# Performance work log

Measured on AMD Instinct MI355X. Metric: run time of the kernel, lower is better.

Reference implementation:

```python
import jax
import jax.numpy as jnp
from jax import lax
import numpy as np

E = 4          # num_experts
CIN = 128
COUT = 128
K = 3
STAT = 6
HID = 16       # router hidden width
STRIDE = 1
PAD = 1


def setup_inputs() -> dict:
    key = jax.random.key(0)
    ks = jax.random.split(key, 8)
    B, H, W = 32, 64, 64
    x = jax.random.normal(ks[0], (B, CIN, H, W), dtype=jnp.float32)
    scene_stats = jax.random.normal(ks[1], (B, STAT), dtype=jnp.float32)
    # router: Linear(stat_dim,16) -> ReLU -> Linear(16,E) -> Softmax
    W1 = jax.random.normal(ks[2], (HID, STAT), dtype=jnp.float32) * (1.0 / np.sqrt(STAT))
    b1 = jnp.zeros((HID,), dtype=jnp.float32)
    W2 = jax.random.normal(ks[3], (E, HID), dtype=jnp.float32) * (1.0 / np.sqrt(HID))
    b2 = jnp.zeros((E,), dtype=jnp.float32)
    weight_experts = jax.random.normal(ks[4], (E, COUT, CIN, K, K), dtype=jnp.float32) * 0.02
    bias_experts = jnp.zeros((E, COUT), dtype=jnp.float32)
    return {"x": x, "scene_stats": scene_stats, "W1": W1, "b1": b1,
            "W2": W2, "b2": b2, "weight_experts": weight_experts,
            "bias_experts": bias_experts}


def reference(x, scene_stats, W1, b1, W2, b2, weight_experts, bias_experts):
    B, Cin, H, W = x.shape
    Cout = weight_experts.shape[1]
    # router
    h = jax.nn.relu(scene_stats @ W1.T + b1)                 # [B, HID]
    routing = jax.nn.softmax(h @ W2.T + b2, axis=1)          # [B, E]
    # per-sample dynamic weights / bias
    dyn_w = jnp.einsum('bk,koihw->boihw', routing, weight_experts)  # [B,Cout,Cin,K,K]
    dyn_b = jnp.einsum('bk,ko->bo', routing, bias_experts)          # [B,Cout]
    # grouped conv with groups = B (each sample uses its own filter bank)
    x_r = x.reshape(1, B * Cin, H, W)
    w_r = dyn_w.reshape(B * Cout, Cin, K, K)
    out = lax.conv_general_dilated(
        x_r, w_r,
        window_strides=(STRIDE, STRIDE),
        padding=((PAD, PAD), (PAD, PAD)),
        feature_group_count=B,
        dimension_numbers=('NCHW', 'OIHW', 'NCHW'))
    out = out.reshape(B, Cout, out.shape[2], out.shape[3])
    return out + dyn_b[:, :, None, None]
```

## Files before the change

kernel.cpp:

```cpp
#include <hip/hip_runtime.h>
#include <hip/hip_bf16.h>


typedef short bf16x8 __attribute__((ext_vector_type(8)));
typedef float f32x4  __attribute__((ext_vector_type(4)));
typedef unsigned u32x4 __attribute__((ext_vector_type(4)));

#define VMWAIT(n) asm volatile("s_waitcnt vmcnt(" #n ")" ::: "memory")
#define LGKM0()   asm volatile("s_waitcnt lgkmcnt(0)" ::: "memory")

static __device__ __forceinline__ unsigned short f2bf(float f) {
    unsigned u = __float_as_uint(f);
    u = u + 0x7FFFu + ((u >> 16) & 1u);
    return (unsigned short)(u >> 16);
}

static __device__ __forceinline__ void gl2lds16(const unsigned short* g, unsigned short* l) {
    __builtin_amdgcn_global_load_lds(
        (const __attribute__((address_space(1))) unsigned int*)g,
        (__attribute__((address_space(3))) unsigned int*)l,
        16, 0, 0);
}

__global__ void prep_kernel(const float* __restrict__ stats, const float* __restrict__ W1,
                            const float* __restrict__ b1, const float* __restrict__ W2,
                            const float* __restrict__ b2, const float* __restrict__ wexp,
                            const float* __restrict__ bexp, unsigned short* __restrict__ dynw,
                            float* __restrict__ dynb)
{
    __shared__ float ls[4*1152];
    __shared__ float lr[32*4];
    const int tid = threadIdx.x;
    const int co  = blockIdx.x & 127;
    const int bg  = blockIdx.x >> 7;

    if (tid < 32) {
        float s[6];
#pragma unroll
        for (int i = 0; i < 6; ++i) s[i] = stats[tid*6 + i];
        float h[16];
#pragma unroll
        for (int j = 0; j < 16; ++j) {
            float a = b1[j];
#pragma unroll
            for (int i = 0; i < 6; ++i) a += W1[j*6+i]*s[i];
            h[j] = a > 0.f ? a : 0.f;
        }
        float lg[4];
#pragma unroll
        for (int e = 0; e < 4; ++e) {
            float a = b2[e];
#pragma unroll
            for (int j = 0; j < 16; ++j) a += W2[e*16+j]*h[j];
            lg[e] = a;
        }
        float m = fmaxf(fmaxf(lg[0],lg[1]), fmaxf(lg[2],lg[3]));
        float ex[4], sum = 0.f;
#pragma unroll
        for (int e = 0; e < 4; ++e) { ex[e] = expf(lg[e]-m); sum += ex[e]; }
        float inv = 1.f / sum;
#pragma unroll
        for (int e = 0; e < 4; ++e) lr[tid*4+e] = ex[e]*inv;
    }
    for (int i = tid; i < 4*1152; i += 256) {
        int e = i / 1152, j = i - e*1152;
        ls[i] = wexp[((unsigned long long)(e*128 + co))*1152 + j];
    }
    __syncthreads();

    if (bg == 0 && tid < 32) {
        float sb = 0.f;
#pragma unroll
        for (int e = 0; e < 4; ++e) sb += lr[tid*4+e] * bexp[e*128 + co];
        dynb[tid*128 + co] = sb;
    }

    const int ci  = tid & 127;
    const int tp0 = tid >> 7;
    const int cic = ci >> 5;
    const int g   = (ci >> 3) & 3;
    const int jj  = ci & 7;
    const int mi  = co >> 4;
    const int l15 = co & 15;
    for (int bb = bg*8; bb < bg*8 + 8; ++bb) {
        float r0 = lr[bb*4+0], r1 = lr[bb*4+1], r2 = lr[bb*4+2], r3 = lr[bb*4+3];
#pragma unroll
        for (int pp = 0; pp < 5; ++pp) {
            int tap = 2*pp + tp0;
            if (tap < 9) {
                int j = ci*9 + tap;
                float v = r0*ls[j] + r1*ls[1152+j] + r2*ls[2*1152+j] + r3*ls[3*1152+j];
                dynw[((((unsigned long long)(bb*4 + cic)*9 + tap)*8 + mi)*64 + g*16 + l15)*8 + jj] = f2bf(v);
            }
        }
    }
}

__global__ __launch_bounds__(256, 2) void conv_kernel(
    const float* __restrict__ x,
    const unsigned short* __restrict__ dynw,
    const float* __restrict__ dynb,
    float* __restrict__ out)
{
    __shared__ __align__(16) unsigned short xs[6*16*136];
    __shared__ __align__(16) unsigned short wsm[6][4096];

    const int tid  = threadIdx.x;
    const int wave = tid >> 6;
    const int lane = tid & 63;
    const int l15  = lane & 15;
    const int g    = lane >> 4;
    const int pr   = tid >> 4;
    const int c4   = tid & 15;

    int bidx = ((blockIdx.x & 7) << 6) | (blockIdx.x >> 3);
    const int b  = bidx >> 4;
    const int r0 = (bidx & 15) << 2;

    f32x4 acc[8][4];
#pragma unroll
    for (int mi = 0; mi < 8; ++mi)
#pragma unroll
        for (int ni = 0; ni < 4; ++ni) acc[mi][ni] = (f32x4){0.f,0.f,0.f,0.f};

    const float* xsrcb = x + (unsigned long long)b*(128ull*64*64);
    const unsigned short* wsrcb = dynw + (unsigned long long)b*(4ull*9*4096);

    float4 xv[6][2];

#define P1ISSUE(CIC_, KK)                                                      \
    do {                                                                       \
        int grow_ = r0 + (KK) - 1;                                             \
        int growc_ = grow_ < 0 ? 0 : (grow_ > 63 ? 63 : grow_);                \
        const float* xp_ = xsrcb + (unsigned)(((CIC_)*32 + 2*pr)*4096)         \
                         + growc_*64 + c4*4;                                   \
        xv[KK][0] = *(const float4*)xp_;                                       \
        xv[KK][1] = *(const float4*)(xp_ + 4096);                              \
    } while (0)

#define P1PROC(KK)                                                             \
    do {                                                                       \
        int grow_ = r0 + (KK) - 1;                                             \
        bool oob_ = (grow_ < 0) || (grow_ > 63);                               \
        float4 va_ = xv[KK][0], vb_ = xv[KK][1];                               \
        unsigned w0_ = oob_ ? 0u : (f2bf(va_.x) | ((unsigned)f2bf(vb_.x) << 16)); \
        unsigned w1_ = oob_ ? 0u : (f2bf(va_.y) | ((unsigned)f2bf(vb_.y) << 16)); \
        unsigned w2_ = oob_ ? 0u : (f2bf(va_.z) | ((unsigned)f2bf(vb_.z) << 16)); \
        unsigned w3_ = oob_ ? 0u : (f2bf(va_.w) | ((unsigned)f2bf(vb_.w) << 16)); \
        *(uint4*)((char*)xs + (KK)*4352 + pr*272 + c4*16)                      \
            = make_uint4(w0_, w1_, w2_, w3_);                                  \
    } while (0)

    if (tid < 96)
        *(uint4*)((char*)xs + (tid >> 4)*4352 + (tid & 15)*272 + 256)
            = make_uint4(0,0,0,0);
    P1ISSUE(0,0); P1ISSUE(0,1); P1ISSUE(0,2);
    P1ISSUE(0,3); P1ISSUE(0,4); P1ISSUE(0,5);
#pragma unroll
    for (int t = 0; t < 3; ++t) {
        const unsigned short* wsrc = wsrcb + (unsigned)(t*4096);
        gl2lds16(wsrc + (unsigned)tid*8,       wsm[t] + (unsigned)tid*8);
        gl2lds16(wsrc + (unsigned)(tid+256)*8, wsm[t] + (unsigned)(tid+256)*8);
    }
    VMWAIT(6);
    P1PROC(0); P1PROC(1); P1PROC(2); P1PROC(3); P1PROC(4); P1PROC(5);
    VMWAIT(0);
    LGKM0();
    __builtin_amdgcn_s_barrier();
    __builtin_amdgcn_sched_barrier(0);

#pragma unroll
    for (int p = 0; p < 12; ++p) {
        if (p > 0) {
            VMWAIT(0);
            __builtin_amdgcn_s_barrier();
            __builtin_amdgcn_sched_barrier(0);
        }
        if ((p % 3) == 0 && p > 0) {
            P1PROC(0); P1PROC(1); P1PROC(2); P1PROC(3); P1PROC(4); P1PROC(5);
            LGKM0();
            __builtin_amdgcn_s_barrier();
            __builtin_amdgcn_sched_barrier(0);
        }
        if (p < 11) {
#pragma unroll
            for (int t = 0; t < 3; ++t) {
                const int s = 3*p + 3 + t;
                const unsigned short* wsrc = wsrcb + (unsigned)(s*4096);
                unsigned short* wd = wsm[s % 6];
                gl2lds16(wsrc + (unsigned)tid*8,       wd + (unsigned)tid*8);
                gl2lds16(wsrc + (unsigned)(tid+256)*8, wd + (unsigned)(tid+256)*8);
            }
        }
        if ((p % 3) == 2 && p < 9) {
            const int nc = p/3 + 1;
            P1ISSUE(nc,0); P1ISSUE(nc,1); P1ISSUE(nc,2);
            P1ISSUE(nc,3); P1ISSUE(nc,4); P1ISSUE(nc,5);
            __builtin_amdgcn_sched_barrier(0);
        }
        const int ky   = p % 3;
        const int lrow = wave + ky;
        __builtin_amdgcn_s_setprio(1);
#pragma unroll
        for (int kx = 0; kx < 3; ++kx) {
            const unsigned short* wb = wsm[(3*p + kx) % 6];
            u32x4 bv[4];
#pragma unroll
            for (int ni = 0; ni < 4; ++ni) {
                int c = 16*ni + l15 + kx - 1;
                int w = (c < 0) ? 65 : c;
                const char* bp = (const char*)xs + lrow*4352 + g*1088 + w*4;
                bv[ni].x = *(const unsigned*)(bp);
                bv[ni].y = *(const unsigned*)(bp + 272);
                bv[ni].z = *(const unsigned*)(bp + 544);
                bv[ni].w = *(const unsigned*)(bp + 816);
            }
#pragma unroll
            for (int mi = 0; mi < 8; ++mi) {
                bf16x8 afrag = *(const bf16x8*)(wb + (unsigned)((mi*64 + lane)*8));
#pragma unroll
                for (int ni = 0; ni < 4; ++ni)
                    acc[mi][ni] = __builtin_amdgcn_mfma_f32_16x16x32_bf16(
                                      afrag, __builtin_bit_cast(bf16x8, bv[ni]),
                                      acc[mi][ni], 0, 0, 0);
            }
        }
        __builtin_amdgcn_s_setprio(0);
    }

    const int y = r0 + wave;
#pragma unroll
    for (int mi = 0; mi < 8; ++mi) {
#pragma unroll
        for (int r = 0; r < 4; ++r) {
            int co = 16*mi + g*4 + r;
            float bias = dynb[b*128 + co];
            float* op = out + (((unsigned long long)(b*128 + co))*64 + y)*64;
#pragma unroll
            for (int ni = 0; ni < 4; ++ni)
                op[16*ni + l15] = acc[mi][ni][r] + bias;
        }
    }
#undef P1PROC
#undef P1ISSUE
}

extern "C" void kernel_launch(void* const* d_in, const int* in_sizes, int n_in,
                              void* d_out, int out_size, void* d_ws, size_t ws_size,
                              hipStream_t stream)
{
    const float* x     = (const float*)d_in[0];
    const float* stats = (const float*)d_in[1];
    const float* W1    = (const float*)d_in[2];
    const float* b1    = (const float*)d_in[3];
    const float* W2    = (const float*)d_in[4];
    const float* b2    = (const float*)d_in[5];
    const float* wexp  = (const float*)d_in[6];
    const float* bexp  = (const float*)d_in[7];
    float* out = (float*)d_out;

    char* ws = (char*)d_ws;
    float* dynb           = (float*)(ws + 512);
    unsigned short* dynw  = (unsigned short*)(ws + 32768);

    prep_kernel<<<512, 256, 0, stream>>>(stats, W1, b1, W2, b2, wexp, bexp, dynw, dynb);
    conv_kernel<<<512, 256, 0, stream>>>(x, dynw, dynb, out);
}
```

Baseline: 59.65 us.

## Transpose x tile in LDS to column-major and split x staging pipeline

The LDS copy of the input tile is re-laid out as [row][column][channel] with an 80-byte column pitch and explicit zero pad columns. Each B fragment then becomes a single 16-byte LDS read instead of four scattered 4-byte reads per MFMA tile. The staging writes become four 4-byte scattered stores, and the x prefetch is split into two groups: two rows packed early at q==2 and four rows at the next chunk start. This spreads register pressure and global-load latency across the pipeline, at the cost of more LDS write instructions and possible bank conflicts on the strided stores.

```diff
diff --git a/kernel.cpp b/kernel.cpp
--- a/kernel.cpp
+++ b/kernel.cpp
@@ -4,7 +4,6 @@
 
 typedef short bf16x8 __attribute__((ext_vector_type(8)));
 typedef float f32x4  __attribute__((ext_vector_type(4)));
-typedef unsigned u32x4 __attribute__((ext_vector_type(4)));
 
 #define VMWAIT(n) asm volatile("s_waitcnt vmcnt(" #n ")" ::: "memory")
 #define LGKM0()   asm volatile("s_waitcnt lgkmcnt(0)" ::: "memory")
@@ -102,7 +101,7 @@
     const float* __restrict__ dynb,
     float* __restrict__ out)
 {
-    __shared__ __align__(16) unsigned short xs[6*16*136];
+    __shared__ __align__(16) unsigned short xs[6*66*40];
     __shared__ __align__(16) unsigned short wsm[6][4096];
 
     const int tid  = threadIdx.x;
@@ -126,36 +125,43 @@
     const float* xsrcb = x + (unsigned long long)b*(128ull*64*64);
     const unsigned short* wsrcb = dynw + (unsigned long long)b*(4ull*9*4096);
 
-    float4 xv[6][2];
-
-#define P1ISSUE(CIC_, KK)                                                      \
+    float4 xvA[2][2];
+    float4 xvB[4][2];
+
+#define XISSUE(CIC_, KK, DST)                                                  \
     do {                                                                       \
         int grow_ = r0 + (KK) - 1;                                             \
         int growc_ = grow_ < 0 ? 0 : (grow_ > 63 ? 63 : grow_);                \
         const float* xp_ = xsrcb + (unsigned)(((CIC_)*32 + 2*pr)*4096)         \
                          + growc_*64 + c4*4;                                   \
-        xv[KK][0] = *(const float4*)xp_;                                       \
-        xv[KK][1] = *(const float4*)(xp_ + 4096);                              \
+        DST[0] = *(const float4*)xp_;                                          \
+        DST[1] = *(const float4*)(xp_ + 4096);                                 \
     } while (0)
 
-#define P1PROC(KK)                                                             \
+#define XPACK(KK, SRC)                                                         \
     do {                                                                       \
         int grow_ = r0 + (KK) - 1;                                             \
         bool oob_ = (grow_ < 0) || (grow_ > 63);                               \
-        float4 va_ = xv[KK][0], vb_ = xv[KK][1];                               \
+        float4 va_ = SRC[0], vb_ = SRC[1];                                     \
         unsigned w0_ = oob_ ? 0u : (f2bf(va_.x) | ((unsigned)f2bf(vb_.x) << 16)); \
         unsigned w1_ = oob_ ? 0u : (f2bf(va_.y) | ((unsigned)f2bf(vb_.y) << 16)); \
         unsigned w2_ = oob_ ? 0u : (f2bf(va_.z) | ((unsigned)f2bf(vb_.z) << 16)); \
         unsigned w3_ = oob_ ? 0u : (f2bf(va_.w) | ((unsigned)f2bf(vb_.w) << 16)); \
-        *(uint4*)((char*)xs + (KK)*4352 + pr*272 + c4*16)                      \
-            = make_uint4(w0_, w1_, w2_, w3_);                                  \
+        char* bp_ = (char*)xs + (KK)*5280 + (4*c4 + 1)*80 + pr*4;              \
+        *(unsigned*)(bp_)       = w0_;                                         \
+        *(unsigned*)(bp_ + 80)  = w1_;                                         \
+        *(unsigned*)(bp_ + 160) = w2_;                                         \
+        *(unsigned*)(bp_ + 240) = w3_;                                         \
     } while (0)
 
-    if (tid < 96)
-        *(uint4*)((char*)xs + (tid >> 4)*4352 + (tid & 15)*272 + 256)
-            = make_uint4(0,0,0,0);
-    P1ISSUE(0,0); P1ISSUE(0,1); P1ISSUE(0,2);
-    P1ISSUE(0,3); P1ISSUE(0,4); P1ISSUE(0,5);
+    if (tid < 60) {
+        int r = tid / 10, rem = tid - r*10;
+        int col = (rem < 5) ? 0 : 65;
+        int qq  = (rem < 5) ? rem : rem - 5;
+        *(uint4*)((char*)xs + r*5280 + col*80 + qq*16) = make_uint4(0,0,0,0);
+    }
+    XISSUE(0,0,xvA[0]); XISSUE(0,1,xvA[1]);
+    XISSUE(0,2,xvB[0]); XISSUE(0,3,xvB[1]); XISSUE(0,4,xvB[2]); XISSUE(0,5,xvB[3]);
 #pragma unroll
     for (int t = 0; t < 3; ++t) {
         const unsigned short* wsrc = wsrcb + (unsigned)(t*4096);
@@ -163,7 +169,8 @@
         gl2lds16(wsrc + (unsigned)(tid+256)*8, wsm[t] + (unsigned)(tid+256)*8);
     }
     VMWAIT(6);
-    P1PROC(0); P1PROC(1); P1PROC(2); P1PROC(3); P1PROC(4); P1PROC(5);
+    XPACK(0,xvA[0]); XPACK(1,xvA[1]);
+    XPACK(2,xvB[0]); XPACK(3,xvB[1]); XPACK(4,xvB[2]); XPACK(5,xvB[3]);
     VMWAIT(0);
     LGKM0();
     __builtin_amdgcn_s_barrier();
@@ -171,13 +178,15 @@
 
 #pragma unroll
     for (int p = 0; p < 12; ++p) {
+        const int cic = p / 3;
+        const int q   = p % 3;
         if (p > 0) {
             VMWAIT(0);
             __builtin_amdgcn_s_barrier();
             __builtin_amdgcn_sched_barrier(0);
         }
-        if ((p % 3) == 0 && p > 0) {
-            P1PROC(0); P1PROC(1); P1PROC(2); P1PROC(3); P1PROC(4); P1PROC(5);
+        if (q == 0 && p > 0) {
+            XPACK(2,xvB[0]); XPACK(3,xvB[1]); XPACK(4,xvB[2]); XPACK(5,xvB[3]);
             LGKM0();
             __builtin_amdgcn_s_barrier();
             __builtin_amdgcn_sched_barrier(0);
@@ -192,28 +201,27 @@
                 gl2lds16(wsrc + (unsigned)(tid+256)*8, wd + (unsigned)(tid+256)*8);
             }
         }
-        if ((p % 3) == 2 && p < 9) {
-            const int nc = p/3 + 1;
-            P1ISSUE(nc,0); P1ISSUE(nc,1); P1ISSUE(nc,2);
-            P1ISSUE(nc,3); P1ISSUE(nc,4); P1ISSUE(nc,5);
-            __builtin_amdgcn_sched_barrier(0);
-        }
-        const int ky   = p % 3;
-        const int lrow = wave + ky;
+        if (q == 1 && cic < 3) {
+            XISSUE(cic+1,0,xvA[0]); XISSUE(cic+1,1,xvA[1]);
+            __builtin_amdgcn_sched_barrier(0);
+        }
+        if (q == 2 && cic < 3) {
+            XPACK(0,xvA[0]); XPACK(1,xvA[1]);
+            XISSUE(cic+1,2,xvB[0]); XISSUE(cic+1,3,xvB[1]);
+            XISSUE(cic+1,4,xvB[2]); XISSUE(cic+1,5,xvB[3]);
+            __builtin_amdgcn_sched_barrier(0);
+        }
+        const int lrow = wave + q;
         __builtin_amdgcn_s_setprio(1);
 #pragma unroll
         for (int kx = 0; kx < 3; ++kx) {
             const unsigned short* wb = wsm[(3*p + kx) % 6];
-            u32x4 bv[4];
+            bf16x8 bfr[4];
 #pragma unroll
             for (int ni = 0; ni < 4; ++ni) {
-                int c = 16*ni + l15 + kx - 1;
-                int w = (c < 0) ? 65 : c;
-                const char* bp = (const char*)xs + lrow*4352 + g*1088 + w*4;
-                bv[ni].x = *(const unsigned*)(bp);
-                bv[ni].y = *(const unsigned*)(bp + 272);
-                bv[ni].z = *(const unsigned*)(bp + 544);
-                bv[ni].w = *(const unsigned*)(bp + 816);
+                int lcol = 16*ni + l15 + kx;
+                bfr[ni] = *(const bf16x8*)((const char*)xs
+                              + lrow*5280 + lcol*80 + g*16);
             }
 #pragma unroll
             for (int mi = 0; mi < 8; ++mi) {
@@ -221,8 +229,7 @@
 #pragma unroll
                 for (int ni = 0; ni < 4; ++ni)
                     acc[mi][ni] = __builtin_amdgcn_mfma_f32_16x16x32_bf16(
-                                      afrag, __builtin_bit_cast(bf16x8, bv[ni]),
-                                      acc[mi][ni], 0, 0, 0);
+                                      afrag, bfr[ni], acc[mi][ni], 0, 0, 0);
             }
         }
         __builtin_amdgcn_s_setprio(0);
@@ -241,8 +248,8 @@
                 op[16*ni + l15] = acc[mi][ni][r] + bias;
         }
     }
-#undef P1PROC
-#undef P1ISSUE
+#undef XPACK
+#undef XISSUE
 }
 
 extern "C" void kernel_launch(void* const* d_in, const int* in_sizes, int n_in,
```

Measured after the change: 58.90 us. About the same (-1.3%).
